# Optimization experiments

Measured on AMD Instinct MI355X. Metric: run time of the kernel, lower is better.

## Reference

```python
import jax, jax.numpy as jnp
import numpy as np

NUM_HEADS = 12
WINDOW = 128
LOOK_B = 1
LOOK_F = 1


def look_around(x, pad_value):
    # x: (b, n_windows, window, ...) ; pad along window axis (axis=1), concat along axis=2
    pads = [(0, 0), (LOOK_B, LOOK_F)] + [(0, 0)] * (x.ndim - 2)
    p = jnp.pad(x, pads, constant_values=pad_value)
    n = x.shape[1]
    return jnp.concatenate([p[:, i:i + n] for i in range(LOOK_B + LOOK_F + 1)], axis=2)


def split_heads(x):
    # (L, B, D) -> (B*H, L, hd), batch-major over heads (index = b*H + h)
    L, B, D = x.shape
    return jnp.transpose(x.reshape(L, B * NUM_HEADS, D // NUM_HEADS), (1, 0, 2))


def merge_heads(x):
    # (B*H, L, hd) -> (L, B, D)
    BH, L, hd = x.shape
    return jnp.transpose(x, (1, 0, 2)).reshape(L, BH // NUM_HEADS, hd * NUM_HEADS)


def setup_inputs() -> dict:
    key = jax.random.key(0)
    ks = jax.random.split(key, 12)
    S, B, D = 4096, 8, 768
    inp = {
        'hidden_states': jax.random.normal(ks[0], (S, B, D), dtype=jnp.float32),
        'key_padding_mask': jax.random.bernoulli(ks[1], 0.2, (B, S)),
    }
    scale = 0.02
    for i, name in enumerate(['Wq', 'Wk', 'Wv', 'Wgq']):
        inp[name] = jax.random.normal(ks[2 + i], (D, D), dtype=jnp.float32) * scale
    for i, name in enumerate(['bq', 'bk', 'bv', 'bgq']):
        inp[name] = jax.random.normal(ks[6 + i], (D,), dtype=jnp.float32) * scale
    return inp


def reference(hidden_states, key_padding_mask, Wq, bq, Wk, bk, Wv, bv, Wgq, bgq):
    S, B, D = hidden_states.shape
    H, W = NUM_HEADS, WINDOW
    hd = D // H
    n = S // W
    BH = B * H
    neg = -jnp.finfo(hidden_states.dtype).max
    inv_sqrt = hd ** (-0.5)

    q = split_heads(hidden_states @ Wq + bq)  # (BH, S, hd)
    k = split_heads(hidden_states @ Wk + bk)
    v = split_heads(hidden_states @ Wv + bv)

    # --- local windowed attention ---
    bq_ = q.reshape(BH, n, W, hd)
    bk_ = look_around(k.reshape(BH, n, W, hd), 0.0)   # (BH, n, 3W, hd)
    bv_ = look_around(v.reshape(BH, n, W, hd), 0.0)
    dots = jnp.einsum('bnie,bnje->bnij', bq_, bk_) * inv_sqrt  # (BH, n, W, 3W)

    im = key_padding_mask.reshape(B, n, W)
    km = look_around(im, True)                        # (B, n, 3W), pads masked
    mask = im[:, :, :, None] | km[:, :, None, :]      # (B, n, W, 3W)
    mask = jnp.broadcast_to(mask[:, None], (B, H, n, W, 3 * W)).reshape(BH, n, W, 3 * W)
    dots = jnp.where(mask, neg, dots)
    attn = jax.nn.softmax(dots, axis=-1)
    out = jnp.einsum('bnij,bnje->bnie', attn, bv_).reshape(BH, S, hd)
    out = merge_heads(out)                            # (S, B, D)

    # --- global-token attention (token 0 attends to everything) ---
    gq = split_heads(hidden_states[0:1] @ Wgq + bgq)  # (BH, 1, hd)
    gdots = jnp.einsum('bie,bje->bij', gq, k) * inv_sqrt  # (BH, 1, S)
    gmask = jnp.broadcast_to(key_padding_mask[:, None], (B, H, S)).reshape(BH, S)
    gdots = jnp.where(gmask[:, None, :], neg, gdots)
    gattn = jax.nn.softmax(gdots, axis=-1)
    gout = merge_heads(jnp.einsum('bij,bje->bie', gattn, v))  # (1, B, D)

    return out.at[0].set(gout[0])
```

## Files before the change

### kernel.cpp

```cpp
#include <hip/hip_runtime.h>
#include <float.h>

#define S_  4096
#define B_  8
#define D_  768
#define H_  12
#define HD_ 64
#define W_  128
#define BH_ 96
#define SB_ 32768

typedef unsigned short u16;
typedef __attribute__((ext_vector_type(8))) short bf16x8;
typedef __attribute__((ext_vector_type(4))) float f32x4;

#define MFMA16(a,b,c) __builtin_amdgcn_mfma_f32_16x16x32_bf16(a,b,c,0,0,0)

__device__ __forceinline__ u16 f2bf(float x){
  unsigned int u = __float_as_uint(x);
  return (u16)((u + 0x7FFFu + ((u >> 16) & 1u)) >> 16);
}
__device__ __forceinline__ float bf2f(unsigned int lo16){ return __uint_as_float(lo16 << 16); }
__device__ __forceinline__ float bflo(unsigned int u){ return __uint_as_float(u << 16); }
__device__ __forceinline__ float bfhi(unsigned int u){ return __uint_as_float(u & 0xFFFF0000u); }
__device__ __forceinline__ unsigned int pk2(float a, float b){
  return (unsigned int)f2bf(a) | ((unsigned int)f2bf(b) << 16);
}

__device__ __forceinline__ void gload_lds16(const void* g, void* l){
  __builtin_amdgcn_global_load_lds(
      (const __attribute__((address_space(1))) void*)g,
      (__attribute__((address_space(3))) void*)l, 16, 0, 0);
}

__device__ __forceinline__ bool mask_at(const void* mp, int flag, int idx){
  return flag ? (((const unsigned char*)mp)[idx] != 0)
              : (((const unsigned int*)mp)[idx] != 0u);
}

__global__ __launch_bounds__(256) void sniff_mask_kernel(const unsigned int* __restrict__ m,
                                                         int* __restrict__ flag){
  __shared__ unsigned int red[256];
  unsigned int acc = 0u;
  for (int i = threadIdx.x; i < 8192; i += 256) acc |= m[i];
  red[threadIdx.x] = acc;
  __syncthreads();
  for (int s = 128; s > 0; s >>= 1){
    if ((int)threadIdx.x < s) red[threadIdx.x] |= red[threadIdx.x + s];
    __syncthreads();
  }
  if (threadIdx.x == 0){
    unsigned int o = red[0];
    *flag = (o > 1u && (o & 0xFEFEFEFEu) == 0u) ? 1 : 0;
  }
}

__global__ __launch_bounds__(256) void cvt_hidden_kernel(const float* __restrict__ src,
                                                         u16* __restrict__ dst){
  int idx = blockIdx.x * 256 + threadIdx.x;
  for (int base = idx * 8; base < 25165824; base += 2048 * 256 * 8){
    float4 a = *(const float4*)&src[base];
    float4 b = *(const float4*)&src[base + 4];
    uint4 o;
    o.x = pk2(a.x, a.y); o.y = pk2(a.z, a.w);
    o.z = pk2(b.x, b.y); o.w = pk2(b.z, b.w);
    *(uint4*)&dst[base] = o;
  }
}

__global__ __launch_bounds__(256) void cvt_wT_kernel(const float* __restrict__ W0,
    const float* __restrict__ W1, const float* __restrict__ W2, u16* __restrict__ wT){
  __shared__ float tile[64][65];
  const float* Wsel = blockIdx.z == 0 ? W0 : (blockIdx.z == 1 ? W1 : W2);
  const int t = threadIdx.x;
  const int kt0 = blockIdx.x * 64, nt0 = blockIdx.y * 64;
  { const int row = t >> 2, c16 = (t & 3) * 16;
#pragma unroll
    for (int j = 0; j < 4; ++j){
      float4 v = *(const float4*)&Wsel[(size_t)(kt0 + row) * 768 + nt0 + c16 + j * 4];
      tile[row][c16 + j*4 + 0] = v.x; tile[row][c16 + j*4 + 1] = v.y;
      tile[row][c16 + j*4 + 2] = v.z; tile[row][c16 + j*4 + 3] = v.w;
    } }
  __syncthreads();
  { const int nl = t >> 2, k16 = (t & 3) * 16;
    unsigned int o[8];
#pragma unroll
    for (int j = 0; j < 8; ++j)
      o[j] = pk2(tile[k16 + 2*j][nl], tile[k16 + 2*j + 1][nl]);
    u16* dst = wT + (size_t)blockIdx.z * 589824 + (size_t)(nt0 + nl) * 768 + kt0 + k16;
    *(uint4*)dst       = make_uint4(o[0], o[1], o[2], o[3]);
    *(uint4*)(dst + 8) = make_uint4(o[4], o[5], o[6], o[7]); }
}

__global__ __launch_bounds__(256) void proj_mfma_kernel(
    const u16* __restrict__ hb, const u16* __restrict__ wT,
    const float* __restrict__ bq, const float* __restrict__ bk, const float* __restrict__ bv,
    u16* __restrict__ qb, u16* __restrict__ kb, u16* __restrict__ vb){
  __shared__ union ShMem {
    struct { u16 A0[8192]; u16 B0[8192]; u16 A1[8192]; u16 B1[8192]; } ab;
    u16 C[128 * 130];
  } sh;
  const int t = threadIdx.x;
  const int id = blockIdx.x;
  const int xcd = id & 7, loc = id >> 3;
  const int nt = loc % 18;
  const int mt = xcd * 32 + loc / 18;
  const int p  = nt / 6;
  const int c0 = (nt % 6) * 128;
  const int r0 = mt * 128;
  const float* bias = p == 0 ? bq : (p == 1 ? bk : bv);
  u16* dst = p == 0 ? qb : (p == 1 ? kb : vb);
  const u16* wTp = wT + (size_t)p * 589824;

  const int lane = t & 63, w = t >> 6;
  const int l15 = lane & 15, lg = lane >> 4;
  const int wr = w >> 1, wc = w & 1;
  const int lrc = lane >> 3, slot = lane & 7;

  f32x4 acc[4][4] = {};

#define PSTAGE(AS, BS, kof) do{ \
    _Pragma("unroll") \
    for (int c = 0; c < 4; ++c){ \
      int chunk = w * 4 + c; \
      int ldsrow = chunk * 8 + lrc; \
      int slotg = slot ^ (ldsrow & 7); \
      gload_lds16(&hb [(size_t)(r0 + ldsrow) * 768 + (kof) + slotg * 8], &AS[chunk * 512]); \
      gload_lds16(&wTp[(size_t)(c0 + ldsrow) * 768 + (kof) + slotg * 8], &BS[chunk * 512]); \
    } \
  }while(0)

#define PITER(AS, BS, kof, VNSTR, DOSTAGE) do{ \
    asm volatile("s_waitcnt vmcnt(" VNSTR ")" ::: "memory"); \
    __builtin_amdgcn_sched_barrier(0); \
    __builtin_amdgcn_s_barrier(); \
    bf16x8 af[4][2], bf[4][2]; \
    _Pragma("unroll") \
    for (int mf = 0; mf < 4; ++mf) \
      _Pragma("unroll") \
      for (int ks = 0; ks < 2; ++ks) \
        af[mf][ks] = *(const bf16x8*)&AS[(wr*64 + mf*16 + l15) * 64 + (((ks*4 + lg) ^ (l15 & 7)) * 8)]; \
    _Pragma("unroll") \
    for (int nf = 0; nf < 4; ++nf) \
      _Pragma("unroll") \
      for (int ks = 0; ks < 2; ++ks) \
        bf[nf][ks] = *(const bf16x8*)&BS[(wc*64 + nf*16 + l15) * 64 + (((ks*4 + lg) ^ (l15 & 7)) * 8)]; \
    asm volatile("s_waitcnt lgkmcnt(0)" ::: "memory"); \
    __builtin_amdgcn_sched_barrier(0); \
    __builtin_amdgcn_s_barrier(); \
    if (DOSTAGE) PSTAGE(AS, BS, (kof) + 128); \
    _Pragma("unroll") \
    for (int ks = 0; ks < 2; ++ks) \
      _Pragma("unroll") \
      for (int mf = 0; mf < 4; ++mf) \
        _Pragma("unroll") \
        for (int nf = 0; nf < 4; ++nf) \
          acc[mf][nf] = MFMA16(af[mf][ks], bf[nf][ks], acc[mf][nf]); \
  }while(0)

  PSTAGE(sh.ab.A0, sh.ab.B0, 0);
  PSTAGE(sh.ab.A1, sh.ab.B1, 64);
  for (int i2 = 0; i2 < 5; ++i2){
    const int kc = i2 * 128;
    PITER(sh.ab.A0, sh.ab.B0, kc,      "8", 1);
    PITER(sh.ab.A1, sh.ab.B1, kc + 64, "8", 1);
  }
  PITER(sh.ab.A0, sh.ab.B0, 640, "8", 0);
  PITER(sh.ab.A1, sh.ab.B1, 704, "0", 0);
#undef PSTAGE
#undef PITER

#pragma unroll
  for (int nf = 0; nf < 4; ++nf){
    int c = c0 + wc*64 + nf*16 + l15;
    float bsv = bias[c];
#pragma unroll
    for (int mf = 0; mf < 4; ++mf)
#pragma unroll
      for (int r = 0; r < 4; ++r)
        sh.C[(wr*64 + mf*16 + lg*4 + r) * 130 + wc*64 + nf*16 + l15] = f2bf(acc[mf][nf][r] + bsv);
  }
  __syncthreads();
  { const int b = t >> 5, hh2 = (t >> 4) & 1, sl = t & 15;
    const int srow0 = r0 >> 3;
    const int hh = (c0 >> 6) + hh2;
    u16* dp = dst + ((size_t)(b * 12 + hh) * 4096 + srow0 + sl) * 64;
    const u16* sp = &sh.C[(sl * 8 + b) * 130 + hh2 * 64];
#pragma unroll
    for (int j = 0; j < 8; ++j)
      *(uint4*)(dp + j*8) = *(const uint4*)(sp + j*8);
  }
}

__global__ __launch_bounds__(256) void vt_kernel(const u16* __restrict__ vb, u16* __restrict__ vtb){
  __shared__ u16 tile[64][72];
  const int t = threadIdx.x;
  const int stile = blockIdx.x, bh = blockIdx.y;
  { const int sl = t >> 2, q = (t & 3) * 16;
    const u16* src = &vb[((size_t)bh * 4096 + stile * 64 + sl) * 64 + q];
    *(uint4*)&tile[sl][q]     = *(const uint4*)src;
    *(uint4*)&tile[sl][q + 8] = *(const uint4*)(src + 8); }
  __syncthreads();
  { const int d = t >> 2, sq = (t & 3) * 16;
    unsigned int o[8];
#pragma unroll
    for (int j = 0; j < 8; ++j){
      unsigned int lo = tile[sq + 2*j][d], hi = tile[sq + 2*j + 1][d];
      o[j] = lo | (hi << 16);
    }
    u16* dst = vtb + ((size_t)bh * 64 + d) * 4096 + stile * 64 + sq;
    *(uint4*)dst       = make_uint4(o[0], o[1], o[2], o[3]);
    *(uint4*)(dst + 8) = make_uint4(o[4], o[5], o[6], o[7]); }
}

__global__ __launch_bounds__(256) void local_mfma_kernel(
    const u16* __restrict__ qb, const u16* __restrict__ kb, const u16* __restrict__ vtb,
    const void* __restrict__ maskp, const int* __restrict__ flagp,
    float* __restrict__ out){
  __shared__ u16 KsA[64 * 64], KsB[64 * 64];
  __shared__ u16 VsA[64 * 64], VsB[64 * 64];
  __shared__ u16 Ps[4][32][72];
  __shared__ float kpen[384];
  __shared__ float qpen_s[128];
  const int t = threadIdx.x;
  const int id = blockIdx.x;
  const int swz = (id & 7) * 384 + (id >> 3);
  const int n_i = swz & 31, bh = swz >> 5;
  const int b_i = bh / 12, h = bh % 12;
  const int flag = *flagp;
  const int w = t >> 6, lane = t & 63, l15 = lane & 15, lg = lane >> 4;
  const int lrc = lane >> 3, slot = lane & 7;
  const int jbase0 = n_i * 128 - 128;
  const int jt_lo = (n_i == 0) ? 2 : 0;
  const int jt_hi = (n_i == 31) ? 4 : 6;

#define STAGE_TILE(KS, VS, jtv) do{ \
    int jb_ = jbase0 + (jtv) * 64; \
    _Pragma("unroll") \
    for (int c = 0; c < 2; ++c){ \
      int chunk = w * 2 + c; \
      int ldsrow = chunk * 8 + lrc; \
      int slotg = slot ^ (ldsrow & 7); \
      gload_lds16(&kb [((size_t)bh * 4096 + jb_ + ldsrow) * 64 + slotg * 8], &KS[chunk * 512]); \
      gload_lds16(&vtb[((size_t)bh * 64 + ldsrow) * 4096 + jb_ + slotg * 8], &VS[chunk * 512]); \
    } \
  }while(0)

#define COMPUTE_TILE(KS, VS, jtv) do{ \
    f32x4 dt[2][4] = {}; \
    __builtin_amdgcn_s_setprio(1); \
    _Pragma("unroll") \
    for (int ks2 = 0; ks2 < 2; ++ks2) \
      _Pragma("unroll") \
      for (int nf = 0; nf < 4; ++nf){ \
        bf16x8 bk_ = *(const bf16x8*)&KS[(nf*16 + l15) * 64 + (((ks2*4 + lg) ^ (l15 & 7)) * 8)]; \
        dt[0][nf] = MFMA16(bk_, aq[0][ks2], dt[0][nf]);    \
        dt[1][nf] = MFMA16(bk_, aq[1][ks2], dt[1][nf]); \
      } \
    __builtin_amdgcn_s_setprio(0); \
     \
    _Pragma("unroll") \
    for (int nf = 0; nf < 4; ++nf){ \
      float4 kpv = *(const float4*)&kpen[(jtv)*64 + nf*16 + lg*4]; \
      _Pragma("unroll") \
      for (int mf = 0; mf < 2; ++mf){ \
        dt[mf][nf][0] = (qp2[mf] + kpv.x == 0.f) ? dt[mf][nf][0] * 0.125f : -FLT_MAX; \
        dt[mf][nf][1] = (qp2[mf] + kpv.y == 0.f) ? dt[mf][nf][1] * 0.125f : -FLT_MAX; \
        dt[mf][nf][2] = (qp2[mf] + kpv.z == 0.f) ? dt[mf][nf][2] * 0.125f : -FLT_MAX; \
        dt[mf][nf][3] = (qp2[mf] + kpv.w == 0.f) ? dt[mf][nf][3] * 0.125f : -FLT_MAX; \
      } \
    } \
    _Pragma("unroll") \
    for (int mf = 0; mf < 2; ++mf){ \
      float tm = dt[mf][0][0]; \
      _Pragma("unroll") \
      for (int nf = 0; nf < 4; ++nf) \
        _Pragma("unroll") \
        for (int r = 0; r < 4; ++r) tm = fmaxf(tm, dt[mf][nf][r]); \
      tm = fmaxf(tm, __shfl_xor(tm, 16)); \
      tm = fmaxf(tm, __shfl_xor(tm, 32)); \
      float mold = mrow[mf]; \
      const bool up = (tm > mold + 8.f);         \
      float mnew = up ? tm : mold; \
      mrow[mf] = mnew; \
      float ps = 0.f; \
      _Pragma("unroll") \
      for (int nf = 0; nf < 4; ++nf) \
        _Pragma("unroll") \
        for (int r = 0; r < 4; ++r){ \
          float pv = __expf(dt[mf][nf][r] - mnew);    \
          ps += pv; \
          Ps[w][mf*16 + l15][nf*16 + lg*4 + r] = f2bf(pv); \
        } \
      float scl_own = up ? __expf(mold - mnew) : 1.0f; \
      ps += __shfl_xor(ps, 16); \
      ps += __shfl_xor(ps, 32); \
      lrow[mf] = lrow[mf] * scl_own + ps; \
      if (__any(up)){                           \
        _Pragma("unroll") \
        for (int r = 0; r < 4; ++r){ \
          float sr = __shfl(scl_own, lg*4 + r);   \
          _Pragma("unroll") \
          for (int nf = 0; nf < 4; ++nf) O[mf][nf][r] *= sr; \
        } \
      } \
    } \
    __builtin_amdgcn_s_setprio(1); \
    _Pragma("unroll") \
    for (int ks2 = 0; ks2 < 2; ++ks2){ \
      bf16x8 ap0 = *(const bf16x8*)&Ps[w][l15]     [ks2*32 + lg*8]; \
      bf16x8 ap1 = *(const bf16x8*)&Ps[w][16 + l15][ks2*32 + lg*8]; \
      _Pragma("unroll") \
      for (int nf = 0; nf < 4; ++nf){ \
        bf16x8 bv_ = *(const bf16x8*)&VS[(nf*16 + l15) * 64 + (((ks2*4 + lg) ^ (l15 & 7)) * 8)]; \
        O[0][nf] = MFMA16(ap0, bv_, O[0][nf]); \
        O[1][nf] = MFMA16(ap1, bv_, O[1][nf]); \
      } \
    } \
    __builtin_amdgcn_s_setprio(0); \
  }while(0)

  if (t < 128) qpen_s[t] = mask_at(maskp, flag, b_i * 4096 + n_i * 128 + t) ? 1.f : 0.f;
  for (int j = t; j < 384; j += 256){
    int jp = jbase0 + j;
    kpen[j] = (jp < 0 || jp >= 4096 || mask_at(maskp, flag, b_i * 4096 + jp)) ? 1.f : 0.f;
  }

  bf16x8 aq[2][2];
#pragma unroll
  for (int mf = 0; mf < 2; ++mf)
#pragma unroll
    for (int ks = 0; ks < 2; ++ks)
      aq[mf][ks] = *(const bf16x8*)&qb[((size_t)bh * 4096 + n_i*128 + w*32 + mf*16 + l15) * 64 + ks*32 + lg*8];

  STAGE_TILE(KsA, VsA, jt_lo);
  __syncthreads();

  float qp2[2];
#pragma unroll
  for (int mf = 0; mf < 2; ++mf)
    qp2[mf] = qpen_s[w*32 + mf*16 + l15];

  f32x4 O[2][4] = {};
  float mrow[2] = { -FLT_MAX, -FLT_MAX };
  float lrow[2] = { 0.f, 0.f };

  for (int base = jt_lo; base < jt_hi; base += 2){
    STAGE_TILE(KsB, VsB, base + 1);
    COMPUTE_TILE(KsA, VsA, base);
    __syncthreads();
    if (base + 2 < jt_hi) STAGE_TILE(KsA, VsA, base + 2);
    COMPUTE_TILE(KsB, VsB, base + 1);
    __syncthreads();
  }
#undef STAGE_TILE
#undef COMPUTE_TILE

  const float noor = (n_i == 0 || n_i == 31) ? 128.f : 0.f;
#pragma unroll
  for (int mf = 0; mf < 2; ++mf){
    float lf = lrow[mf] + ((mrow[mf] <= -FLT_MAX) ? noor : 0.f);
    float inv_own = 1.f / lf;
#pragma unroll
    for (int r = 0; r < 4; ++r){
      float inv = __shfl(inv_own, lg*4 + r);
      int srow = n_i*128 + w*32 + mf*16 + lg*4 + r;
      float* op = &out[(size_t)srow * (8 * 768) + b_i * 768 + h * 64];
#pragma unroll
      for (int nf = 0; nf < 4; ++nf)
        op[nf*16 + l15] = O[mf][nf][r] * inv;
    }
  }
}

__global__ __launch_bounds__(256) void gq_kernel(const float* __restrict__ hid,
    const float* __restrict__ Wgq, const float* __restrict__ bgq, float* __restrict__ gq){
  __shared__ float hs[768];
  __shared__ float red[256];
  const int t = threadIdx.x, bh = blockIdx.x, b_i = bh / 12, h = bh % 12;
  for (int c = t; c < 768; c += 256) hs[c] = hid[(size_t)b_i * 768 + c];
  __syncthreads();
  const int dd = t & 63, part = t >> 6;
  float acc = 0.f;
  for (int c = part * 192; c < part * 192 + 192; ++c)
    acc += hs[c] * Wgq[(size_t)c * 768 + h * 64 + dd];
  red[t] = acc;
  __syncthreads();
  if (t < 64)
    gq[bh * 64 + t] = (red[t] + red[t+64] + red[t+128] + red[t+192] + bgq[h*64 + t]) * 0.125f;
}

__global__ __launch_bounds__(256) void gpart_kernel(const float* __restrict__ gq,
    const u16* __restrict__ kb, const u16* __restrict__ vb,
    const void* __restrict__ maskp, const int* __restrict__ flagp,
    float* __restrict__ gp_out){
  __shared__ float gqs[64];
  __shared__ float sc[512];
  __shared__ float red[256];
  const int t = threadIdx.x, bh = blockIdx.x, chunk = blockIdx.y;
  const int b_i = bh / 12;
  const int flag = *flagp;
  if (t < 64) gqs[t] = gq[bh * 64 + t];
  __syncthreads();
#pragma unroll
  for (int i = 0; i < 2; ++i){
    int sl = i * 256 + t;
    int s = chunk * 512 + sl;
    const uint4* kr = (const uint4*)&kb[((size_t)bh * 4096 + s) * 64];
    float dot = 0.f;
#pragma unroll
    for (int u = 0; u < 8; ++u){
      uint4 x = kr[u];
      dot += gqs[u*8+0]*bflo(x.x) + gqs[u*8+1]*bfhi(x.x);
      dot += gqs[u*8+2]*bflo(x.y) + gqs[u*8+3]*bfhi(x.y);
      dot += gqs[u*8+4]*bflo(x.z) + gqs[u*8+5]*bfhi(x.z);
      dot += gqs[u*8+6]*bflo(x.w) + gqs[u*8+7]*bfhi(x.w);
    }
    sc[sl] = mask_at(maskp, flag, b_i * 4096 + s) ? -FLT_MAX : dot;
  }
  __syncthreads();
  float m = fmaxf(sc[t], sc[t + 256]);
  red[t] = m; __syncthreads();
  for (int st = 128; st > 0; st >>= 1){ if (t < st) red[t] = fmaxf(red[t], red[t + st]); __syncthreads(); }
  const float mc = red[0];
  __syncthreads();
  float ls = 0.f;
#pragma unroll
  for (int i = 0; i < 2; ++i){
    int sl = i * 256 + t;
    float p = __expf(sc[sl] - mc);
    sc[sl] = p; ls += p;
  }
  red[t] = ls; __syncthreads();
  for (int st = 128; st > 0; st >>= 1){ if (t < st) red[t] += red[t + st]; __syncthreads(); }
  const float lc = red[0];
  __syncthreads();
  const int dd = t & 63, part = t >> 6;
  float o = 0.f;
  for (int i2 = 0; i2 < 128; ++i2){
    int sl = part * 128 + i2;
    o += sc[sl] * bf2f(vb[((size_t)bh * 4096 + chunk * 512 + sl) * 64 + dd]);
  }
  red[t] = o; __syncthreads();
  float* gp = gp_out + ((size_t)bh * 8 + chunk) * 66;
  if (t == 0){ gp[0] = mc; gp[1] = lc; }
  if (t < 64) gp[2 + t] = red[t] + red[t+64] + red[t+128] + red[t+192];
}

__global__ __launch_bounds__(64) void greduce_kernel(const float* __restrict__ gp_in,
                                                     float* __restrict__ out){
  const int t = threadIdx.x, bh = blockIdx.x, b_i = bh / 12, h = bh % 12;
  const float* gp = gp_in + (size_t)bh * 8 * 66;
  float mg = -FLT_MAX;
#pragma unroll
  for (int c = 0; c < 8; ++c) mg = fmaxf(mg, gp[c * 66]);
  float lg = 0.f, o = 0.f;
#pragma unroll
  for (int c = 0; c < 8; ++c){
    float wv = __expf(gp[c * 66] - mg);
    lg += gp[c * 66 + 1] * wv;
    o  += gp[c * 66 + 2 + t] * wv;
  }
  out[(size_t)b_i * 768 + h * 64 + t] = o / lg;
}

extern "C" void kernel_launch(void* const* d_in, const int* in_sizes, int n_in,
                              void* d_out, int out_size, void* d_ws, size_t ws_size,
                              hipStream_t stream) {
  const float* hid   = (const float*)d_in[0];
  const void*  maskp = d_in[1];
  const float* Wq  = (const float*)d_in[2];
  const float* Wk  = (const float*)d_in[3];
  const float* Wv  = (const float*)d_in[4];
  const float* Wgq = (const float*)d_in[5];
  const float* bq  = (const float*)d_in[6];
  const float* bk  = (const float*)d_in[7];
  const float* bv  = (const float*)d_in[8];
  const float* bgq = (const float*)d_in[9];
  float* out = (float*)d_out;

  char* wsb = (char*)d_ws;
  int* flag   = (int*)wsb;
  u16* hb     = (u16*)(wsb + 256);
  u16* wT     = (u16*)(wsb + 50331904);
  u16* qb     = (u16*)(wsb + 53870848);
  u16* kb     = (u16*)(wsb + 104202496);
  u16* vb     = (u16*)(wsb + 154534144);
  u16* vtb    = (u16*)(wsb + 204865792);
  float* gq   = (float*)(wsb + 255197440);
  float* gpart = (float*)(wsb + 255222016);

  sniff_mask_kernel<<<1, 256, 0, stream>>>((const unsigned int*)maskp, flag);
  cvt_hidden_kernel<<<2048, 256, 0, stream>>>(hid, hb);
  cvt_wT_kernel<<<dim3(12, 12, 3), 256, 0, stream>>>(Wq, Wk, Wv, wT);
  proj_mfma_kernel<<<4608, 256, 0, stream>>>(hb, wT, bq, bk, bv, qb, kb, vb);
  vt_kernel<<<dim3(64, 96), 256, 0, stream>>>(vb, vtb);
  gq_kernel<<<96, 256, 0, stream>>>(hid, Wgq, bgq, gq);
  local_mfma_kernel<<<3072, 256, 0, stream>>>(qb, kb, vtb, maskp, flag, out);
  gpart_kernel<<<dim3(96, 8), 256, 0, stream>>>(gq, kb, vb, maskp, flag, gpart);
  greduce_kernel<<<96, 64, 0, stream>>>(gpart, out);
}
```

Measured before the change: 367.7 us.

## Fuse prep kernels, emit V transpose from projection, fold gq into gpart

Merges the mask sniff, hidden conversion and weight transpose into one launch, partitioned by block index. The projection kernel now also writes the transposed V tile from its shared-memory staging buffer, which removes the separate vt_kernel pass that re-read V from memory. The gq matvec is folded into gpart, where each of the 8 chunks recomputes it redundantly. The aim is fewer launches and less memory traffic, at the cost of redundant gq work and extra strided stores in the projection epilogue.

Result: no change. 367.9 us (+0.1%).

```diff
diff --git a/kernel.cpp b/kernel.cpp
--- a/kernel.cpp
+++ b/kernel.cpp
@@ -38,64 +38,66 @@
               : (((const unsigned int*)mp)[idx] != 0u);
 }
 
-__global__ __launch_bounds__(256) void sniff_mask_kernel(const unsigned int* __restrict__ m,
-                                                         int* __restrict__ flag){
-  __shared__ unsigned int red[256];
-  unsigned int acc = 0u;
-  for (int i = threadIdx.x; i < 8192; i += 256) acc |= m[i];
-  red[threadIdx.x] = acc;
-  __syncthreads();
-  for (int s = 128; s > 0; s >>= 1){
-    if ((int)threadIdx.x < s) red[threadIdx.x] |= red[threadIdx.x + s];
+__global__ __launch_bounds__(256) void prep_kernel(
+    const float* __restrict__ hid, const float* __restrict__ W0,
+    const float* __restrict__ W1, const float* __restrict__ W2,
+    const unsigned int* __restrict__ maskw,
+    u16* __restrict__ hb, u16* __restrict__ wT, int* __restrict__ flag){
+  __shared__ float tile[64][65];
+  const int bid = blockIdx.x, t = threadIdx.x;
+  if (bid < 2048){
+    int idx = bid * 256 + t;
+    for (int base = idx * 8; base < 25165824; base += 2048 * 256 * 8){
+      float4 a = *(const float4*)&hid[base];
+      float4 b = *(const float4*)&hid[base + 4];
+      uint4 o;
+      o.x = pk2(a.x, a.y); o.y = pk2(a.z, a.w);
+      o.z = pk2(b.x, b.y); o.w = pk2(b.z, b.w);
+      *(uint4*)&hb[base] = o;
+    }
+  } else if (bid < 2480){
+    const int wb = bid - 2048;
+    const int mat = wb / 144, r2 = wb % 144;
+    const int kt0 = (r2 / 12) * 64, nt0 = (r2 % 12) * 64;
+    const float* Wsel = mat == 0 ? W0 : (mat == 1 ? W1 : W2);
+    { const int row = t >> 2, c16 = (t & 3) * 16;
+#pragma unroll
+      for (int j = 0; j < 4; ++j){
+        float4 v = *(const float4*)&Wsel[(size_t)(kt0 + row) * 768 + nt0 + c16 + j * 4];
+        tile[row][c16 + j*4 + 0] = v.x; tile[row][c16 + j*4 + 1] = v.y;
+        tile[row][c16 + j*4 + 2] = v.z; tile[row][c16 + j*4 + 3] = v.w;
+      } }
     __syncthreads();
-  }
-  if (threadIdx.x == 0){
-    unsigned int o = red[0];
-    *flag = (o > 1u && (o & 0xFEFEFEFEu) == 0u) ? 1 : 0;
-  }
-}
-
-__global__ __launch_bounds__(256) void cvt_hidden_kernel(const float* __restrict__ src,
-                                                         u16* __restrict__ dst){
-  int idx = blockIdx.x * 256 + threadIdx.x;
-  for (int base = idx * 8; base < 25165824; base += 2048 * 256 * 8){
-    float4 a = *(const float4*)&src[base];
-    float4 b = *(const float4*)&src[base + 4];
-    uint4 o;
-    o.x = pk2(a.x, a.y); o.y = pk2(a.z, a.w);
-    o.z = pk2(b.x, b.y); o.w = pk2(b.z, b.w);
-    *(uint4*)&dst[base] = o;
-  }
-}
-
-__global__ __launch_bounds__(256) void cvt_wT_kernel(const float* __restrict__ W0,
-    const float* __restrict__ W1, const float* __restrict__ W2, u16* __restrict__ wT){
-  __shared__ float tile[64][65];
-  const float* Wsel = blockIdx.z == 0 ? W0 : (blockIdx.z == 1 ? W1 : W2);
-  const int t = threadIdx.x;
-  const int kt0 = blockIdx.x * 64, nt0 = blockIdx.y * 64;
-  { const int row = t >> 2, c16 = (t & 3) * 16;
-#pragma unroll
-    for (int j = 0; j < 4; ++j){
-      float4 v = *(const float4*)&Wsel[(size_t)(kt0 + row) * 768 + nt0 + c16 + j * 4];
-      tile[row][c16 + j*4 + 0] = v.x; tile[row][c16 + j*4 + 1] = v.y;
-      tile[row][c16 + j*4 + 2] = v.z; tile[row][c16 + j*4 + 3] = v.w;
-    } }
-  __syncthreads();
-  { const int nl = t >> 2, k16 = (t & 3) * 16;
-    unsigned int o[8];
-#pragma unroll
-    for (int j = 0; j < 8; ++j)
-      o[j] = pk2(tile[k16 + 2*j][nl], tile[k16 + 2*j + 1][nl]);
-    u16* dst = wT + (size_t)blockIdx.z * 589824 + (size_t)(nt0 + nl) * 768 + kt0 + k16;
-    *(uint4*)dst       = make_uint4(o[0], o[1], o[2], o[3]);
-    *(uint4*)(dst + 8) = make_uint4(o[4], o[5], o[6], o[7]); }
+    { const int nl = t >> 2, k16 = (t & 3) * 16;
+      unsigned int o[8];
+#pragma unroll
+      for (int j = 0; j < 8; ++j)
+        o[j] = pk2(tile[k16 + 2*j][nl], tile[k16 + 2*j + 1][nl]);
+      u16* dst = wT + (size_t)mat * 589824 + (size_t)(nt0 + nl) * 768 + kt0 + k16;
+      *(uint4*)dst       = make_uint4(o[0], o[1], o[2], o[3]);
+      *(uint4*)(dst + 8) = make_uint4(o[4], o[5], o[6], o[7]); }
+  } else {
+    unsigned int* red = (unsigned int*)&tile[0][0];
+    unsigned int acc = 0u;
+    for (int i = t; i < 8192; i += 256) acc |= maskw[i];
+    red[t] = acc;
+    __syncthreads();
+    for (int s = 128; s > 0; s >>= 1){
+      if (t < s) red[t] |= red[t + s];
+      __syncthreads();
+    }
+    if (t == 0){
+      unsigned int o = red[0];
+      *flag = (o > 1u && (o & 0xFEFEFEFEu) == 0u) ? 1 : 0;
+    }
+  }
 }
 
 __global__ __launch_bounds__(256) void proj_mfma_kernel(
     const u16* __restrict__ hb, const u16* __restrict__ wT,
     const float* __restrict__ bq, const float* __restrict__ bk, const float* __restrict__ bv,
-    u16* __restrict__ qb, u16* __restrict__ kb, u16* __restrict__ vb){
+    u16* __restrict__ qb, u16* __restrict__ kb, u16* __restrict__ vb,
+    u16* __restrict__ vtb){
   __shared__ union ShMem {
     struct { u16 A0[8192]; u16 B0[8192]; u16 A1[8192]; u16 B1[8192]; } ab;
     u16 C[128 * 130];
@@ -190,27 +192,24 @@
     for (int j = 0; j < 8; ++j)
       *(uint4*)(dp + j*8) = *(const uint4*)(sp + j*8);
   }
-}
-
-__global__ __launch_bounds__(256) void vt_kernel(const u16* __restrict__ vb, u16* __restrict__ vtb){
-  __shared__ u16 tile[64][72];
-  const int t = threadIdx.x;
-  const int stile = blockIdx.x, bh = blockIdx.y;
-  { const int sl = t >> 2, q = (t & 3) * 16;
-    const u16* src = &vb[((size_t)bh * 4096 + stile * 64 + sl) * 64 + q];
-    *(uint4*)&tile[sl][q]     = *(const uint4*)src;
-    *(uint4*)&tile[sl][q + 8] = *(const uint4*)(src + 8); }
-  __syncthreads();
-  { const int d = t >> 2, sq = (t & 3) * 16;
-    unsigned int o[8];
-#pragma unroll
-    for (int j = 0; j < 8; ++j){
-      unsigned int lo = tile[sq + 2*j][d], hi = tile[sq + 2*j + 1][d];
-      o[j] = lo | (hi << 16);
-    }
-    u16* dst = vtb + ((size_t)bh * 64 + d) * 4096 + stile * 64 + sq;
-    *(uint4*)dst       = make_uint4(o[0], o[1], o[2], o[3]);
-    *(uint4*)(dst + 8) = make_uint4(o[4], o[5], o[6], o[7]); }
+  if (p == 2){
+    const int ri0 = t * 4;
+#pragma unroll
+    for (int j = 0; j < 4; ++j){
+      const int ri = ri0 + j;
+      const int b = ri >> 7, hh2 = (ri >> 6) & 1, dd = ri & 63;
+      unsigned int o[8];
+#pragma unroll
+      for (int q = 0; q < 8; ++q){
+        unsigned int lo = sh.C[((2*q    )*8 + b) * 130 + hh2*64 + dd];
+        unsigned int hi = sh.C[((2*q + 1)*8 + b) * 130 + hh2*64 + dd];
+        o[q] = lo | (hi << 16);
+      }
+      u16* dp2 = vtb + ((size_t)((b*12 + (c0 >> 6) + hh2) * 64) + dd) * 4096 + (r0 >> 3);
+      *(uint4*)dp2       = make_uint4(o[0], o[1], o[2], o[3]);
+      *(uint4*)(dp2 + 8) = make_uint4(o[4], o[5], o[6], o[7]);
+    }
+  }
 }
 
 __global__ __launch_bounds__(256) void local_mfma_kernel(
@@ -373,35 +372,31 @@
   }
 }
 
-__global__ __launch_bounds__(256) void gq_kernel(const float* __restrict__ hid,
-    const float* __restrict__ Wgq, const float* __restrict__ bgq, float* __restrict__ gq){
-  __shared__ float hs[768];
-  __shared__ float red[256];
-  const int t = threadIdx.x, bh = blockIdx.x, b_i = bh / 12, h = bh % 12;
-  for (int c = t; c < 768; c += 256) hs[c] = hid[(size_t)b_i * 768 + c];
-  __syncthreads();
-  const int dd = t & 63, part = t >> 6;
-  float acc = 0.f;
-  for (int c = part * 192; c < part * 192 + 192; ++c)
-    acc += hs[c] * Wgq[(size_t)c * 768 + h * 64 + dd];
-  red[t] = acc;
-  __syncthreads();
-  if (t < 64)
-    gq[bh * 64 + t] = (red[t] + red[t+64] + red[t+128] + red[t+192] + bgq[h*64 + t]) * 0.125f;
-}
-
-__global__ __launch_bounds__(256) void gpart_kernel(const float* __restrict__ gq,
+__global__ __launch_bounds__(256) void gpart_kernel(
+    const float* __restrict__ hid, const float* __restrict__ Wgq, const float* __restrict__ bgq,
     const u16* __restrict__ kb, const u16* __restrict__ vb,
     const void* __restrict__ maskp, const int* __restrict__ flagp,
     float* __restrict__ gp_out){
+  __shared__ float hs[768];
   __shared__ float gqs[64];
   __shared__ float sc[512];
   __shared__ float red[256];
   const int t = threadIdx.x, bh = blockIdx.x, chunk = blockIdx.y;
-  const int b_i = bh / 12;
+  const int b_i = bh / 12, h = bh % 12;
   const int flag = *flagp;
-  if (t < 64) gqs[t] = gq[bh * 64 + t];
-  __syncthreads();
+
+  for (int c = t; c < 768; c += 256) hs[c] = hid[(size_t)b_i * 768 + c];
+  __syncthreads();
+  { const int dd = t & 63, part = t >> 6;
+    float acc = 0.f;
+    for (int c = part * 192; c < part * 192 + 192; ++c)
+      acc += hs[c] * Wgq[(size_t)c * 768 + h * 64 + dd];
+    red[t] = acc; }
+  __syncthreads();
+  if (t < 64)
+    gqs[t] = (red[t] + red[t+64] + red[t+128] + red[t+192] + bgq[h*64 + t]) * 0.125f;
+  __syncthreads();
+
 #pragma unroll
   for (int i = 0; i < 2; ++i){
     int sl = i * 256 + t;
@@ -487,16 +482,12 @@
   u16* kb     = (u16*)(wsb + 104202496);
   u16* vb     = (u16*)(wsb + 154534144);
   u16* vtb    = (u16*)(wsb + 204865792);
-  float* gq   = (float*)(wsb + 255197440);
   float* gpart = (float*)(wsb + 255222016);
 
-  sniff_mask_kernel<<<1, 256, 0, stream>>>((const unsigned int*)maskp, flag);
-  cvt_hidden_kernel<<<2048, 256, 0, stream>>>(hid, hb);
-  cvt_wT_kernel<<<dim3(12, 12, 3), 256, 0, stream>>>(Wq, Wk, Wv, wT);
-  proj_mfma_kernel<<<4608, 256, 0, stream>>>(hb, wT, bq, bk, bv, qb, kb, vb);
-  vt_kernel<<<dim3(64, 96), 256, 0, stream>>>(vb, vtb);
-  gq_kernel<<<96, 256, 0, stream>>>(hid, Wgq, bgq, gq);
+  prep_kernel<<<2481, 256, 0, stream>>>(hid, Wq, Wk, Wv,
+                                        (const unsigned int*)maskp, hb, wT, flag);
+  proj_mfma_kernel<<<4608, 256, 0, stream>>>(hb, wT, bq, bk, bv, qb, kb, vb, vtb);
   local_mfma_kernel<<<3072, 256, 0, stream>>>(qb, kb, vtb, maskp, flag, out);
-  gpart_kernel<<<dim3(96, 8), 256, 0, stream>>>(gq, kb, vb, maskp, flag, gpart);
+  gpart_kernel<<<dim3(96, 8), 256, 0, stream>>>(hid, Wgq, bgq, kb, vb, maskp, flag, gpart);
   greduce_kernel<<<96, 64, 0, stream>>>(gpart, out);
 }
```
